# Kernel optimization log

Measured on AMD Instinct MI355X. Metric: run time of the kernel, lower is better.

Reference implementation:

```python
import jax, jax.numpy as jnp
import numpy as np

EMB_DIM = 128
DEC_DIM = 128
NEG_INF = -1e10


def setup_inputs() -> dict:
    key = jax.random.key(0)
    k1, k2, k3, k4, k5, k6 = jax.random.split(key, 6)
    B, S = 64, 4096
    hidden = jax.random.normal(k1, (B, DEC_DIM), dtype=jnp.float32)
    seq_embs = jax.random.normal(k2, (S, B, EMB_DIM), dtype=jnp.float32)
    mask = jax.random.randint(k3, (B, S), 0, 2, dtype=jnp.int32)
    # nn.Linear(emb_dim + dec_dim, dec_dim): weight [dec_dim, emb_dim+dec_dim]
    fan_in = EMB_DIM + DEC_DIM
    bound = 1.0 / np.sqrt(fan_in)
    W_attn = jax.random.uniform(k4, (DEC_DIM, fan_in), minval=-bound, maxval=bound, dtype=jnp.float32)
    b_attn = jax.random.uniform(k5, (DEC_DIM,), minval=-bound, maxval=bound, dtype=jnp.float32)
    # nn.Linear(dec_dim, 1, bias=False): weight [1, dec_dim]
    bound_v = 1.0 / np.sqrt(DEC_DIM)
    v_w = jax.random.uniform(k6, (1, DEC_DIM), minval=-bound_v, maxval=bound_v, dtype=jnp.float32)
    return {"hidden": hidden, "seq_embs": seq_embs, "mask": mask,
            "W_attn": W_attn, "b_attn": b_attn, "v_w": v_w}


def reference(hidden, seq_embs, mask, W_attn, b_attn, v_w):
    # hidden: [B, Dd]; seq_embs: [S, B, De]; mask: [B, S]
    # Concat order in torch is (hidden, seq_embs) -> split W accordingly.
    Wh = W_attn[:, :DEC_DIM]   # [Dd, Dd] applied to hidden
    We = W_attn[:, DEC_DIM:]   # [Dd, De] applied to seq_embs
    embs = jnp.transpose(seq_embs, (1, 0, 2))            # [B, S, De]
    # energy = tanh(Linear(cat(hidden, embs))) without materializing concat
    h_proj = hidden @ Wh.T + b_attn                       # [B, Dd]
    e_proj = jnp.einsum('bse,de->bsd', embs, We)          # [B, S, Dd]
    energy = jnp.tanh(h_proj[:, None, :] + e_proj)        # [B, S, Dd]
    attention = jnp.einsum('bsd,d->bs', energy, v_w[0])   # [B, S]
    attention = jnp.where(mask == 0, NEG_INF, attention)
    return jax.nn.softmax(attention, axis=1)
```

## Files before the change

### kernel.cpp

```cpp
#include <hip/hip_runtime.h>
#include <hip/hip_bf16.h>

#define BB 64
#define SS 4096
#define EE 128
#define DD 128
#define FAN 256
#define NEG_INF_F (-1e10f)

typedef __bf16 bf16x8 __attribute__((ext_vector_type(8)));
typedef unsigned short u16x8 __attribute__((ext_vector_type(8)));
typedef float f32x4 __attribute__((ext_vector_type(4)));

__device__ inline bf16x8 ld_frag(const unsigned short* p) {
    union { u16x8 u; bf16x8 b; } c;
    c.u = *(const u16x8*)p;
    return c.b;
}

__device__ inline uint2 f4_to_bf4(float4 f) {
    union { __hip_bfloat162 b; unsigned u; } lo, hi;
    lo.b = __float22bfloat162_rn(make_float2(f.x, f.y));
    hi.b = __float22bfloat162_rn(make_float2(f.z, f.w));
    return make_uint2(lo.u, hi.u);
}

__device__ inline float tanh_fast(float x) {
    float ax = fabsf(x);
    float e = __expf(-2.0f * ax);
    float t = (1.0f - e) * __builtin_amdgcn_rcpf(1.0f + e);
    return x < 0.0f ? -t : t;
}

__global__ __launch_bounds__(256) void prep_kernel(
        const float* __restrict__ hidden, const float* __restrict__ W_attn,
        const float* __restrict__ b_attn, const float* __restrict__ v_w,
        float* __restrict__ hproj, unsigned short* __restrict__ Wb,
        float* __restrict__ v_out) {
    const int b = blockIdx.x;
    const int t = threadIdx.x;
    if (t < 128) {
        float acc = b_attn[t];
        const float* hrow = hidden + b * DD;
        const float* wrow = W_attn + t * FAN;
        #pragma unroll 8
        for (int e = 0; e < DD; e++) acc += hrow[e] * wrow[e];
        hproj[b * DD + t] = acc;
        if (b == 0) v_out[t] = v_w[t];
    } else {
        int tt = t - 128;
        int d  = 2 * b + (tt >> 6);
        int e0 = (tt & 63) * 2;
        float2 src = *(const float2*)(W_attn + d * FAN + DD + e0);
        union { __hip_bfloat162 bb; unsigned u; } c;
        c.bb = __float22bfloat162_rn(src);
        *(unsigned*)&Wb[d * EE + e0] = c.u;
    }
}

__global__ __launch_bounds__(256) void logits_kernel(
        const float* __restrict__ seq_embs, const int* __restrict__ mask,
        const float* __restrict__ hproj, const unsigned short* __restrict__ Wb,
        const float* __restrict__ v, float* __restrict__ logits) {
    __shared__ __attribute__((aligned(16))) unsigned short Xs[64][136];
    __shared__ __attribute__((aligned(16))) unsigned short Ws[128][136];
    __shared__ int   mrow[64];
    __shared__ float hp_s[128];
    __shared__ float v_s[128];

    const int b   = blockIdx.y;
    const int s0  = blockIdx.x * 64;
    const int tid = threadIdx.x;

    const int* __restrict__ mask_g = mask + (size_t)b * SS + s0;

    int mk[4];
    #pragma unroll
    for (int k = 0; k < 4; k++) mk[k] = mask_g[(tid + k * 256) >> 4];

    const float* xbase = seq_embs + (size_t)s0 * (BB * EE) + (size_t)b * EE;
    #pragma unroll
    for (int k = 0; k < 4; k++) {
        const int i = tid + k * 256;
        const int s = i >> 4, e8 = i & 15;
        uint4 o = make_uint4(0u, 0u, 0u, 0u);
        if (mk[k] != 0) {
            const float4* src = (const float4*)(xbase + (size_t)s * (BB * EE) + e8 * 8);
            float4 f0 = src[0], f1 = src[1];
            uint2 a = f4_to_bf4(f0), bq = f4_to_bf4(f1);
            o = make_uint4(a.x, a.y, bq.x, bq.y);
        }
        *(uint4*)&Xs[s][e8 * 8] = o;
    }

    const uint4* __restrict__ Wb16 = (const uint4*)Wb;
    #pragma unroll
    for (int k = 0; k < 8; k++) {
        const int i = tid + k * 256;
        const int d = i >> 4, e8 = i & 15;
        *(uint4*)&Ws[d][e8 * 8] = Wb16[i];
    }

    if (tid < 64) {
        mrow[tid] = mask_g[tid];
    } else if (tid < 192) {
        hp_s[tid - 64] = hproj[b * DD + (tid - 64)];
    } else {
        v_s[tid - 192] = v[tid - 192];
        v_s[tid - 128] = v[tid - 128];
    }
    __syncthreads();

    const int wave = tid >> 6;
    const int lane = tid & 63;
    const int m    = lane & 15;
    const int quad = lane >> 4;

    f32x4 acc[8];
    #pragma unroll
    for (int t = 0; t < 8; t++) acc[t] = (f32x4){0.f, 0.f, 0.f, 0.f};

    const int arow = wave * 16 + m;
    #pragma unroll
    for (int kk = 0; kk < 4; kk++) {
        const int k0 = kk * 32 + quad * 8;
        bf16x8 a = ld_frag(&Xs[arow][k0]);
        #pragma unroll
        for (int t = 0; t < 8; t++) {
            bf16x8 bf = ld_frag(&Ws[t * 16 + m][k0]);
            acc[t] = __builtin_amdgcn_mfma_f32_16x16x32_bf16(a, bf, acc[t], 0, 0, 0);
        }
    }

    float red[4];
    #pragma unroll
    for (int r = 0; r < 4; r++) {
        float part = 0.f;
        #pragma unroll
        for (int t = 0; t < 8; t++) {
            int d = t * 16 + m;
            part += v_s[d] * tanh_fast(hp_s[d] + acc[t][r]);
        }
        part += __shfl_xor(part, 1);
        part += __shfl_xor(part, 2);
        part += __shfl_xor(part, 4);
        part += __shfl_xor(part, 8);
        red[r] = part;
    }
    if (m == 0) {
        #pragma unroll
        for (int r = 0; r < 4; r++) {
            int sl = wave * 16 + quad * 4 + r;
            float val = (mrow[sl] != 0) ? red[r] : NEG_INF_F;
            logits[(size_t)b * SS + s0 + sl] = val;
        }
    }
}

__global__ __launch_bounds__(256) void softmax_kernel(float* __restrict__ logits) {
    const int b = blockIdx.x;
    const int tid = threadIdx.x;
    const int wave = tid >> 6;
    const int lane = tid & 63;
    float* row = logits + (size_t)b * SS;

    float4 vals[4];
    float lmax = -1e30f;
    #pragma unroll
    for (int i = 0; i < 4; i++) {
        vals[i] = *(const float4*)(row + (size_t)(i * 256 + tid) * 4);
        lmax = fmaxf(lmax, fmaxf(fmaxf(vals[i].x, vals[i].y), fmaxf(vals[i].z, vals[i].w)));
    }
    #pragma unroll
    for (int off = 32; off >= 1; off >>= 1)
        lmax = fmaxf(lmax, __shfl_xor(lmax, off));

    __shared__ float smax[4], ssum[4];
    if (lane == 0) smax[wave] = lmax;
    __syncthreads();
    const float gmax = fmaxf(fmaxf(smax[0], smax[1]), fmaxf(smax[2], smax[3]));

    float lsum = 0.f;
    #pragma unroll
    for (int i = 0; i < 4; i++) {
        vals[i].x = __expf(vals[i].x - gmax);
        vals[i].y = __expf(vals[i].y - gmax);
        vals[i].z = __expf(vals[i].z - gmax);
        vals[i].w = __expf(vals[i].w - gmax);
        lsum += (vals[i].x + vals[i].y) + (vals[i].z + vals[i].w);
    }
    #pragma unroll
    for (int off = 32; off >= 1; off >>= 1)
        lsum += __shfl_xor(lsum, off);
    if (lane == 0) ssum[wave] = lsum;
    __syncthreads();
    const float total = (ssum[0] + ssum[1]) + (ssum[2] + ssum[3]);
    const float inv = 1.0f / total;

    #pragma unroll
    for (int i = 0; i < 4; i++) {
        float4 o;
        o.x = vals[i].x * inv; o.y = vals[i].y * inv;
        o.z = vals[i].z * inv; o.w = vals[i].w * inv;
        *(float4*)(row + (size_t)(i * 256 + tid) * 4) = o;
    }
}

extern "C" void kernel_launch(void* const* d_in, const int* in_sizes, int n_in,
                              void* d_out, int out_size, void* d_ws, size_t ws_size,
                              hipStream_t stream) {
    const float* hidden   = (const float*)d_in[0];
    const float* seq_embs = (const float*)d_in[1];
    const int*   mask     = (const int*)d_in[2];
    const float* W_attn   = (const float*)d_in[3];
    const float* b_attn   = (const float*)d_in[4];
    const float* v_w      = (const float*)d_in[5];
    float* out = (float*)d_out;

    float*          hproj = (float*)d_ws;
    unsigned short* Wb    = (unsigned short*)((char*)d_ws + 32768);
    float*          vv    = (float*)((char*)d_ws + 65536);

    prep_kernel<<<64, 256, 0, stream>>>(hidden, W_attn, b_attn, v_w, hproj, Wb, vv);
    dim3 grid(SS / 64, BB);
    logits_kernel<<<grid, 256, 0, stream>>>(seq_embs, mask, hproj, Wb, vv, out);
    softmax_kernel<<<BB, 256, 0, stream>>>(out);
}
```

Measured before the change: 224.1 us.

## Load A fragments directly from global into registers, skip masked tanh work

```diff
diff --git a/kernel.cpp b/kernel.cpp
--- a/kernel.cpp
+++ b/kernel.cpp
@@ -62,35 +62,34 @@
         const float* __restrict__ seq_embs, const int* __restrict__ mask,
         const float* __restrict__ hproj, const unsigned short* __restrict__ Wb,
         const float* __restrict__ v, float* __restrict__ logits) {
-    __shared__ __attribute__((aligned(16))) unsigned short Xs[64][136];
     __shared__ __attribute__((aligned(16))) unsigned short Ws[128][136];
-    __shared__ int   mrow[64];
-    __shared__ float hp_s[128];
-    __shared__ float v_s[128];
-
-    const int b   = blockIdx.y;
-    const int s0  = blockIdx.x * 64;
-    const int tid = threadIdx.x;
+
+    const int b    = blockIdx.y;
+    const int s0   = blockIdx.x * 64;
+    const int tid  = threadIdx.x;
+    const int wave = tid >> 6;
+    const int lane = tid & 63;
+    const int m    = lane & 15;
+    const int quad = lane >> 4;
 
     const int* __restrict__ mask_g = mask + (size_t)b * SS + s0;
 
-    int mk[4];
-    #pragma unroll
-    for (int k = 0; k < 4; k++) mk[k] = mask_g[(tid + k * 256) >> 4];
-
-    const float* xbase = seq_embs + (size_t)s0 * (BB * EE) + (size_t)b * EE;
-    #pragma unroll
-    for (int k = 0; k < 4; k++) {
-        const int i = tid + k * 256;
-        const int s = i >> 4, e8 = i & 15;
-        uint4 o = make_uint4(0u, 0u, 0u, 0u);
-        if (mk[k] != 0) {
-            const float4* src = (const float4*)(xbase + (size_t)s * (BB * EE) + e8 * 8);
-            float4 f0 = src[0], f1 = src[1];
+    const int arow = wave * 16 + m;
+    const int am   = mask_g[arow];
+    const float* xrow = seq_embs + (size_t)(s0 + arow) * (BB * EE)
+                      + (size_t)b * EE + quad * 8;
+    bf16x8 afrag[4];
+    #pragma unroll
+    for (int kk = 0; kk < 4; kk++) {
+        union { uint4 q; bf16x8 bf; } c;
+        c.q = make_uint4(0u, 0u, 0u, 0u);
+        if (am != 0) {
+            float4 f0 = *(const float4*)(xrow + kk * 32);
+            float4 f1 = *(const float4*)(xrow + kk * 32 + 4);
             uint2 a = f4_to_bf4(f0), bq = f4_to_bf4(f1);
-            o = make_uint4(a.x, a.y, bq.x, bq.y);
+            c.q = make_uint4(a.x, a.y, bq.x, bq.y);
         }
-        *(uint4*)&Xs[s][e8 * 8] = o;
+        afrag[kk] = c.bf;
     }
 
     const uint4* __restrict__ Wb16 = (const uint4*)Wb;
@@ -100,60 +99,48 @@
         const int d = i >> 4, e8 = i & 15;
         *(uint4*)&Ws[d][e8 * 8] = Wb16[i];
     }
-
-    if (tid < 64) {
-        mrow[tid] = mask_g[tid];
-    } else if (tid < 192) {
-        hp_s[tid - 64] = hproj[b * DD + (tid - 64)];
-    } else {
-        v_s[tid - 192] = v[tid - 192];
-        v_s[tid - 128] = v[tid - 128];
-    }
     __syncthreads();
 
-    const int wave = tid >> 6;
-    const int lane = tid & 63;
-    const int m    = lane & 15;
-    const int quad = lane >> 4;
-
     f32x4 acc[8];
     #pragma unroll
     for (int t = 0; t < 8; t++) acc[t] = (f32x4){0.f, 0.f, 0.f, 0.f};
-
-    const int arow = wave * 16 + m;
     #pragma unroll
     for (int kk = 0; kk < 4; kk++) {
         const int k0 = kk * 32 + quad * 8;
-        bf16x8 a = ld_frag(&Xs[arow][k0]);
         #pragma unroll
         for (int t = 0; t < 8; t++) {
             bf16x8 bf = ld_frag(&Ws[t * 16 + m][k0]);
-            acc[t] = __builtin_amdgcn_mfma_f32_16x16x32_bf16(a, bf, acc[t], 0, 0, 0);
+            acc[t] = __builtin_amdgcn_mfma_f32_16x16x32_bf16(afrag[kk], bf, acc[t], 0, 0, 0);
         }
     }
+
+    float hp_r[8], v_r[8];
+    #pragma unroll
+    for (int t = 0; t < 8; t++) {
+        hp_r[t] = hproj[b * DD + t * 16 + m];
+        v_r[t]  = v[t * 16 + m];
+    }
+    const int4 mq = *(const int4*)(mask_g + wave * 16 + quad * 4);
+    const int mqa[4] = {mq.x, mq.y, mq.z, mq.w};
 
     float red[4];
     #pragma unroll
     for (int r = 0; r < 4; r++) {
         float part = 0.f;
-        #pragma unroll
-        for (int t = 0; t < 8; t++) {
-            int d = t * 16 + m;
-            part += v_s[d] * tanh_fast(hp_s[d] + acc[t][r]);
+        if (mqa[r] != 0) {
+            #pragma unroll
+            for (int t = 0; t < 8; t++)
+                part += v_r[t] * tanh_fast(hp_r[t] + acc[t][r]);
+            part += __shfl_xor(part, 1);
+            part += __shfl_xor(part, 2);
+            part += __shfl_xor(part, 4);
+            part += __shfl_xor(part, 8);
         }
-        part += __shfl_xor(part, 1);
-        part += __shfl_xor(part, 2);
-        part += __shfl_xor(part, 4);
-        part += __shfl_xor(part, 8);
-        red[r] = part;
+        red[r] = (mqa[r] != 0) ? part : NEG_INF_F;
     }
     if (m == 0) {
-        #pragma unroll
-        for (int r = 0; r < 4; r++) {
-            int sl = wave * 16 + quad * 4 + r;
-            float val = (mrow[sl] != 0) ? red[r] : NEG_INF_F;
-            logits[(size_t)b * SS + s0 + sl] = val;
-        }
+        float4 o = make_float4(red[0], red[1], red[2], red[3]);
+        *(float4*)&logits[(size_t)b * SS + s0 + wave * 16 + quad * 4] = o;
     }
 }
 
```

New measurement: 220.9 us. No clear change (-1.4%).
